# Kernel tuning notes

Hardware: AMD Instinct MI355X
Metric: run time of the kernel (lower is better)

Reference implementation:

```python
import jax, jax.numpy as jnp
import numpy as np

B, C, H, W = 16, 1, 128, 8192
N_MAX = 128
CHIRP_W, PERIOD = 48, 64
W_OUT = N_MAX * CHIRP_W + (N_MAX - 1)  # 6271 compacted columns (chirps + separators)
SEP_CLASS_ID = 2


def setup_inputs() -> dict:
    key = jax.random.key(0)
    k1, k2, k3, k4 = jax.random.split(key, 4)
    x = jax.random.normal(k1, (B, C, H, W), dtype=jnp.float32)
    starts = jnp.arange(N_MAX, dtype=jnp.int32) * PERIOD
    xi = jnp.stack([starts, starts + CHIRP_W], axis=-1)           # (N_MAX, 2)
    xi = jnp.broadcast_to(xi[None], (B, N_MAX, 2)).astype(jnp.int32)
    N = jax.random.randint(k2, (B,), 96, N_MAX + 1, dtype=jnp.int32)
    N = N.at[0].set(N_MAX)  # pin so static W_OUT equals torch's dynamic int(w_max.max())
    xl = jax.random.randint(k3, (B, W), 0, 2, dtype=jnp.int32)
    sep_param = jax.random.normal(k4, (1, 1, 1), dtype=jnp.float32)
    return {"x": x, "xi": xi, "N": N, "xl": xl, "sep_param": sep_param, "w_out": W_OUT}


def _compactify(x, xi, N, xl, sep_param, w_out):
    """Vectorized TinyBird.compactify_data: remove silence, keep chirp blocks,
    insert one separator column between consecutive valid chirps."""
    Bx, Cx, Hx, Wx = x.shape
    n_max = xi.shape[1]
    idx = jnp.arange(n_max, dtype=jnp.int32)[None, :]             # (1, N_max)
    Nb = N.reshape(-1, 1).astype(jnp.int32)
    valid = idx < Nb                                              # (B, N_max)

    s0, e0 = xi[..., 0], xi[..., 1]
    w = jnp.clip(e0 - s0, 0, None)
    w_valid = jnp.where(valid, w, 0)
    csum = jnp.cumsum(w_valid, axis=1)
    sn = csum - w_valid + idx                                     # new start (seps before = idx)
    en = csum + idx                                               # new end
    xi_new = jnp.where(valid[..., None], jnp.stack([sn, en], -1), 0).astype(xi.dtype)

    BIG = jnp.int32(1 << 30)
    en_srt = jnp.where(valid, en, BIG)                            # strictly increasing over valid part
    t = jnp.arange(w_out, dtype=jnp.int32)[None, :]               # (1, w_out)
    # i = number of chirp ends <= t  ->  chirp whose [sn_i, en_i) may contain t
    i = (en_srt[:, :, None] <= t[:, None, :]).sum(axis=1).astype(jnp.int32)  # (B, w_out)
    ic = jnp.clip(i, 0, n_max - 1)
    take = lambda a: jnp.take_along_axis(a, ic, axis=1)
    sn_i, en_i = take(sn), take(en)
    s0_i, e0_i = take(s0), take(e0)
    in_chirp = (i < Nb) & (t >= sn_i) & (en_i > sn_i) & (e0_i > s0_i)
    src = jnp.clip(s0_i + (t - sn_i), 0, Wx - 1)                  # (B, w_out)

    # separator column: t == en_{i-1}, previous chirp is not the last valid one, en < W
    jp = jnp.clip(i - 1, 0, n_max - 1)
    en_prev = jnp.take_along_axis(en, jp, axis=1)
    is_sep = (i >= 1) & (t == en_prev) & ((i - 1) < (Nb - 1)) & (en_prev < Wx)

    x_g = jnp.take_along_axis(x, src[:, None, None, :], axis=3)   # (B, C, H, w_out)
    sep = sep_param[0, 0, 0]
    x_new = jnp.where(in_chirp[:, None, None, :], x_g,
                      jnp.where(is_sep[:, None, None, :], sep, jnp.float32(0)))
    xl_g = jnp.take_along_axis(xl, src, axis=1)
    xl_new = jnp.where(in_chirp, xl_g,
                       jnp.where(is_sep, jnp.asarray(SEP_CLASS_ID, xl.dtype),
                                 jnp.asarray(0, xl.dtype)))
    return x_new, xi_new, xl_new


def reference(x, xi, N, xl, sep_param, w_out):
    return _compactify(x, xi, N, xl, sep_param, w_out)
```

## Files before the change

### kernel.cpp

```cpp
#include <hip/hip_runtime.h>

#define BB     16
#define HH     128
#define WW     8192
#define N_MAXC 128
#define W_OUTC 6271
#define SEP_CLASS 2.0f

#define X_ELEMS (BB * HH * W_OUTC)
#define XI_OFF  (X_ELEMS)
#define XL_OFF  (X_ELEMS + BB * N_MAXC * 2)
#define NCHUNKS (X_ELEMS / 4)

#define MAP_BYTES ((size_t)(BB * W_OUTC) * sizeof(int))

#define GBLK  1568
#define GSTR  (GBLK * 256)
#define GITER 8

#define MTILE 512

__global__ __launch_bounds__(256) void tb_meta(const int* __restrict__ xi,
                                               const int* __restrict__ Nv,
                                               const int* __restrict__ xl,
                                               float* __restrict__ out,
                                               int* __restrict__ map) {
    __shared__ int s_s0[N_MAXC], s_e0[N_MAXC], s_scan[N_MAXC], s_sn[N_MAXC], s_en[N_MAXC];
    const int b   = blockIdx.x;
    const int tid = threadIdx.x;
    const int Nb  = Nv[b];

    int wv = 0;
    if (tid < N_MAXC) {
        int2 se = ((const int2*)xi)[b * N_MAXC + tid];
        s_s0[tid] = se.x; s_e0[tid] = se.y;
        int w = se.y - se.x; if (w < 0) w = 0;
        wv = (tid < Nb) ? w : 0;
        s_scan[tid] = wv;
    }
    __syncthreads();
    #pragma unroll
    for (int off = 1; off < N_MAXC; off <<= 1) {
        int v = 0;
        if (tid < N_MAXC && tid >= off) v = s_scan[tid - off];
        __syncthreads();
        if (tid < N_MAXC) s_scan[tid] += v;
        __syncthreads();
    }
    if (tid < N_MAXC) {
        int c = s_scan[tid];
        s_sn[tid] = c - wv + tid;
        s_en[tid] = c + tid;
    }
    __syncthreads();

    if (blockIdx.y == 0 && tid < N_MAXC) {
        const bool valid = tid < Nb;
        out[XI_OFF + (b * N_MAXC + tid) * 2 + 0] = valid ? (float)s_sn[tid] : 0.0f;
        out[XI_OFF + (b * N_MAXC + tid) * 2 + 1] = valid ? (float)s_en[tid] : 0.0f;
    }

    const int t_lo = blockIdx.y * MTILE;
    const int t_hi = (t_lo + MTILE < W_OUTC) ? t_lo + MTILE : W_OUTC;
    for (int t = t_lo + tid; t < t_hi; t += 256) {
        int lo = 0, hi = Nb;
        while (lo < hi) { int mid = (lo + hi) >> 1; if (s_en[mid] <= t) lo = mid + 1; else hi = mid; }
        const int i  = lo;
        const int ic = (i < N_MAXC - 1) ? i : (N_MAXC - 1);
        int m = -2;
        if (i < Nb) {
            int sn = s_sn[ic], en = s_en[ic];
            if (t >= sn && en > sn && s_e0[ic] > s_s0[ic]) {
                int src = s_s0[ic] + (t - sn);
                src = src < 0 ? 0 : (src > WW - 1 ? WW - 1 : src);
                m = src;
            }
        }
        if (m == -2 && i >= 1) {
            int ep = s_en[i - 1];
            if (t == ep && (i - 1) < (Nb - 1) && ep < WW) m = -1;
        }
        if (map) map[b * W_OUTC + t] = m;
        float v = (m >= 0) ? (float)xl[b * WW + m] : ((m == -1) ? SEP_CLASS : 0.0f);
        out[XL_OFF + b * W_OUTC + t] = v;
    }
}

__global__ __launch_bounds__(256) void tb_gather_flat(const float* __restrict__ x,
                                                      const int* __restrict__ map,
                                                      const float* __restrict__ sep_param,
                                                      float* __restrict__ out) {
    const unsigned gtid = blockIdx.x * 256u + threadIdx.x;
    const float sep = sep_param[0];

    unsigned rowA[GITER], colA[GITER];
    int      mv[GITER][4];
    float    xv[GITER][4];

    #pragma unroll
    for (int j = 0; j < GITER; ++j) {
        unsigned c = gtid + (unsigned)j * (unsigned)GSTR;
        if (c >= (unsigned)NCHUNKS) c = NCHUNKS - 1;
        const unsigned flat = c * 4u;
        const unsigned bh   = flat / (unsigned)W_OUTC;
        rowA[j] = bh;
        colA[j] = flat - bh * (unsigned)W_OUTC;
    }
    #pragma unroll
    for (int j = 0; j < GITER; ++j) {
        #pragma unroll
        for (int k = 0; k < 4; ++k) {
            unsigned tk = colA[j] + (unsigned)k;
            unsigned r  = rowA[j];
            if (tk >= (unsigned)W_OUTC) { tk -= (unsigned)W_OUTC; r += 1u; }
            mv[j][k] = map[(r >> 7) * (unsigned)W_OUTC + tk];
        }
    }
    #pragma unroll
    for (int j = 0; j < GITER; ++j) {
        #pragma unroll
        for (int k = 0; k < 4; ++k) {
            unsigned tk = colA[j] + (unsigned)k;
            unsigned r  = rowA[j];
            if (tk >= (unsigned)W_OUTC) r += 1u;
            const int m = mv[j][k];
            const unsigned a = (m >= 0) ? (unsigned)m : 0u;
            xv[j][k] = x[((size_t)r << 13) + a];
        }
    }
    #pragma unroll
    for (int j = 0; j < GITER; ++j) {
        const unsigned c = gtid + (unsigned)j * (unsigned)GSTR;
        if (c < (unsigned)NCHUNKS) {
            float4 v;
            v.x = (mv[j][0] >= 0) ? xv[j][0] : ((mv[j][0] == -1) ? sep : 0.0f);
            v.y = (mv[j][1] >= 0) ? xv[j][1] : ((mv[j][1] == -1) ? sep : 0.0f);
            v.z = (mv[j][2] >= 0) ? xv[j][2] : ((mv[j][2] == -1) ? sep : 0.0f);
            v.w = (mv[j][3] >= 0) ? xv[j][3] : ((mv[j][3] == -1) ? sep : 0.0f);
            ((float4*)out)[c] = v;
        }
    }
}

#define FTILE   512
#define FHCHUNK 32

__global__ __launch_bounds__(256) void tb_gather_tiled(const float* __restrict__ x,
                                                       const int* __restrict__ xi,
                                                       const int* __restrict__ Nv,
                                                       const float* __restrict__ sep_param,
                                                       float* __restrict__ out) {
    __shared__ int s_s0[N_MAXC], s_e0[N_MAXC], s_sn[N_MAXC], s_en[N_MAXC];
    __shared__ int s_map[FTILE];
    const int b = blockIdx.z, h0 = blockIdx.y * FHCHUNK, t0 = blockIdx.x * FTILE;
    const int tid = threadIdx.x, Nb = Nv[b];
    if (tid < N_MAXC) {
        s_s0[tid] = xi[(b * N_MAXC + tid) * 2 + 0];
        s_e0[tid] = xi[(b * N_MAXC + tid) * 2 + 1];
    }
    __syncthreads();
    if (tid == 0) {
        int c = 0;
        for (int i = 0; i < N_MAXC; ++i) {
            int w = s_e0[i] - s_s0[i]; if (w < 0) w = 0;
            int wvv = (i < Nb) ? w : 0;
            c += wvv;
            s_sn[i] = c - wvv + i;
            s_en[i] = c + i;
        }
    }
    __syncthreads();
    for (int j = tid; j < FTILE; j += 256) {
        int t = t0 + j, m = -2;
        if (t < W_OUTC) {
            int lo = 0, hi = Nb;
            while (lo < hi) { int mid = (lo + hi) >> 1; if (s_en[mid] <= t) lo = mid + 1; else hi = mid; }
            int i = lo, ic = (i < N_MAXC - 1) ? i : (N_MAXC - 1);
            if (i < Nb) {
                int sn = s_sn[ic], en = s_en[ic];
                if (t >= sn && en > sn && s_e0[ic] > s_s0[ic]) {
                    int src = s_s0[ic] + (t - sn);
                    m = src < 0 ? 0 : (src > WW - 1 ? WW - 1 : src);
                }
            }
            if (m == -2 && i >= 1) {
                int ep = s_en[i - 1];
                if (t == ep && (i - 1) < (Nb - 1) && ep < WW) m = -1;
            }
        }
        s_map[j] = m;
    }
    __syncthreads();
    const float sep = sep_param[0];
    const float* xb = x + (size_t)b * HH * WW;
    float* ob = out + (size_t)b * HH * W_OUTC;
    for (int r = 0; r < FHCHUNK; ++r) {
        const int h = h0 + r;
        const float* xr = xb + (size_t)h * WW;
        float* orow = ob + (size_t)h * W_OUTC;
        for (int j = tid; j < FTILE; j += 256) {
            int t = t0 + j;
            if (t < W_OUTC) {
                int m = s_map[j];
                orow[t] = (m >= 0) ? xr[m] : ((m == -1) ? sep : 0.0f);
            }
        }
    }
}

extern "C" void kernel_launch(void* const* d_in, const int* in_sizes, int n_in,
                              void* d_out, int out_size, void* d_ws, size_t ws_size,
                              hipStream_t stream) {
    const float* x   = (const float*)d_in[0];
    const int*   xi  = (const int*)  d_in[1];
    const int*   Nv  = (const int*)  d_in[2];
    const int*   xl  = (const int*)  d_in[3];
    const float* sep = (const float*)d_in[4];
    float*       out = (float*)d_out;

    const bool use_ws = (ws_size >= MAP_BYTES) && (d_ws != nullptr);
    int* map = use_ws ? (int*)d_ws : nullptr;

    tb_meta<<<dim3(BB, 13), dim3(256), 0, stream>>>(xi, Nv, xl, out, map);

    if (use_ws) {
        tb_gather_flat<<<dim3(GBLK), dim3(256), 0, stream>>>(x, map, sep, out);
    } else {
        dim3 grid((W_OUTC + FTILE - 1) / FTILE, HH / FHCHUNK, BB);
        tb_gather_tiled<<<grid, dim3(256), 0, stream>>>(x, xi, Nv, sep, out);
    }
}
```

Before: 135.6 us.

## Stage per-batch column map in LDS and gather per batch with nontemporal stores

Replaces the flat grid-strided gather with a kernel launched over a (chunk, batch) grid. Each block copies its batch's column map into shared memory with vector loads, then reads map entries from LDS instead of global memory. The map row is padded to 6272 so the vector copy stays aligned, and output is written with nontemporal float4 stores. The aim is to cut repeated global map traffic and cache pollution from streaming writes, at the cost of about 25 KB of LDS per block, which may limit occupancy.

New measurement: 127.2 us. -6.2%, faster.

```diff
diff --git a/kernel.cpp b/kernel.cpp
--- a/kernel.cpp
+++ b/kernel.cpp
@@ -5,20 +5,25 @@
 #define WW     8192
 #define N_MAXC 128
 #define W_OUTC 6271
+#define MROW   6272
 #define SEP_CLASS 2.0f
 
 #define X_ELEMS (BB * HH * W_OUTC)
 #define XI_OFF  (X_ELEMS)
 #define XL_OFF  (X_ELEMS + BB * N_MAXC * 2)
-#define NCHUNKS (X_ELEMS / 4)
-
-#define MAP_BYTES ((size_t)(BB * W_OUTC) * sizeof(int))
-
-#define GBLK  1568
-#define GSTR  (GBLK * 256)
-#define GITER 8
+
+#define BATCH_ELEMS  (HH * W_OUTC)
+#define BATCH_CHUNKS (BATCH_ELEMS / 4)
+#define RPB   128
+#define CPB   1568
+#define KPT   7
+
+#define MAP_BYTES ((size_t)(BB * MROW) * sizeof(int))
 
 #define MTILE 512
+
+typedef float  vf4 __attribute__((ext_vector_type(4)));
+typedef int    vi4 __attribute__((ext_vector_type(4)));
 
 __global__ __launch_bounds__(256) void tb_meta(const int* __restrict__ xi,
                                                const int* __restrict__ Nv,
@@ -80,64 +85,76 @@
             int ep = s_en[i - 1];
             if (t == ep && (i - 1) < (Nb - 1) && ep < WW) m = -1;
         }
-        if (map) map[b * W_OUTC + t] = m;
+        if (map) map[b * MROW + t] = m;
         float v = (m >= 0) ? (float)xl[b * WW + m] : ((m == -1) ? SEP_CLASS : 0.0f);
         out[XL_OFF + b * W_OUTC + t] = v;
     }
 }
 
-__global__ __launch_bounds__(256) void tb_gather_flat(const float* __restrict__ x,
-                                                      const int* __restrict__ map,
-                                                      const float* __restrict__ sep_param,
-                                                      float* __restrict__ out) {
-    const unsigned gtid = blockIdx.x * 256u + threadIdx.x;
+__global__ __launch_bounds__(256) void tb_gather_lds(const float* __restrict__ x,
+                                                     const int* __restrict__ map,
+                                                     const float* __restrict__ sep_param,
+                                                     float* __restrict__ out) {
+    __shared__ __align__(16) int s_map[MROW];
+    const int b   = blockIdx.y;
+    const int r   = blockIdx.x;
+    const int tid = threadIdx.x;
+
+    const vi4* msrc = (const vi4*)(map + (size_t)b * MROW);
+    #pragma unroll
+    for (int k = 0; k < 7; ++k) {
+        int idx = tid + k * 256;
+        if (idx < MROW / 4) ((vi4*)s_map)[idx] = msrc[idx];
+    }
+    __syncthreads();
+
     const float sep = sep_param[0];
-
-    unsigned rowA[GITER], colA[GITER];
-    int      mv[GITER][4];
-    float    xv[GITER][4];
-
-    #pragma unroll
-    for (int j = 0; j < GITER; ++j) {
-        unsigned c = gtid + (unsigned)j * (unsigned)GSTR;
-        if (c >= (unsigned)NCHUNKS) c = NCHUNKS - 1;
-        const unsigned flat = c * 4u;
-        const unsigned bh   = flat / (unsigned)W_OUTC;
-        rowA[j] = bh;
-        colA[j] = flat - bh * (unsigned)W_OUTC;
-    }
-    #pragma unroll
-    for (int j = 0; j < GITER; ++j) {
+    const int   c0  = r * CPB;
+    const float* xb = x   + ((size_t)b << 20);
+    float*       ob = out + (size_t)b * BATCH_ELEMS;
+
+    unsigned hh[KPT], tt[KPT];
+    int   mv[KPT][4];
+    float xv[KPT][4];
+    bool  act[KPT];
+
+    #pragma unroll
+    for (int k = 0; k < KPT; ++k) {
+        int cl = c0 + tid + k * 256;
+        act[k] = (tid + k * 256 < CPB) && (cl < BATCH_CHUNKS);
+        if (!act[k]) cl = 0;
+        const unsigned e = (unsigned)cl * 4u;
+        const unsigned h = e / (unsigned)W_OUTC;
+        const unsigned t = e - h * (unsigned)W_OUTC;
+        hh[k] = h; tt[k] = t;
         #pragma unroll
-        for (int k = 0; k < 4; ++k) {
-            unsigned tk = colA[j] + (unsigned)k;
-            unsigned r  = rowA[j];
-            if (tk >= (unsigned)W_OUTC) { tk -= (unsigned)W_OUTC; r += 1u; }
-            mv[j][k] = map[(r >> 7) * (unsigned)W_OUTC + tk];
-        }
-    }
-    #pragma unroll
-    for (int j = 0; j < GITER; ++j) {
+        for (int kk = 0; kk < 4; ++kk) {
+            unsigned tk = t + (unsigned)kk;
+            if (tk >= (unsigned)W_OUTC) tk -= (unsigned)W_OUTC;
+            mv[k][kk] = s_map[tk];
+        }
+    }
+    #pragma unroll
+    for (int k = 0; k < KPT; ++k) {
         #pragma unroll
-        for (int k = 0; k < 4; ++k) {
-            unsigned tk = colA[j] + (unsigned)k;
-            unsigned r  = rowA[j];
-            if (tk >= (unsigned)W_OUTC) r += 1u;
-            const int m = mv[j][k];
+        for (int kk = 0; kk < 4; ++kk) {
+            unsigned tk = tt[k] + (unsigned)kk;
+            unsigned h  = hh[k] + ((tk >= (unsigned)W_OUTC) ? 1u : 0u);
+            const int m = mv[k][kk];
             const unsigned a = (m >= 0) ? (unsigned)m : 0u;
-            xv[j][k] = x[((size_t)r << 13) + a];
-        }
-    }
-    #pragma unroll
-    for (int j = 0; j < GITER; ++j) {
-        const unsigned c = gtid + (unsigned)j * (unsigned)GSTR;
-        if (c < (unsigned)NCHUNKS) {
-            float4 v;
-            v.x = (mv[j][0] >= 0) ? xv[j][0] : ((mv[j][0] == -1) ? sep : 0.0f);
-            v.y = (mv[j][1] >= 0) ? xv[j][1] : ((mv[j][1] == -1) ? sep : 0.0f);
-            v.z = (mv[j][2] >= 0) ? xv[j][2] : ((mv[j][2] == -1) ? sep : 0.0f);
-            v.w = (mv[j][3] >= 0) ? xv[j][3] : ((mv[j][3] == -1) ? sep : 0.0f);
-            ((float4*)out)[c] = v;
+            xv[k][kk] = xb[((size_t)h << 13) + a];
+        }
+    }
+    #pragma unroll
+    for (int k = 0; k < KPT; ++k) {
+        if (act[k]) {
+            const int cl = c0 + tid + k * 256;
+            vf4 v;
+            v.x = (mv[k][0] >= 0) ? xv[k][0] : ((mv[k][0] == -1) ? sep : 0.0f);
+            v.y = (mv[k][1] >= 0) ? xv[k][1] : ((mv[k][1] == -1) ? sep : 0.0f);
+            v.z = (mv[k][2] >= 0) ? xv[k][2] : ((mv[k][2] == -1) ? sep : 0.0f);
+            v.w = (mv[k][3] >= 0) ? xv[k][3] : ((mv[k][3] == -1) ? sep : 0.0f);
+            __builtin_nontemporal_store(v, ((vf4*)ob) + cl);
         }
     }
 }
@@ -224,7 +241,7 @@
     tb_meta<<<dim3(BB, 13), dim3(256), 0, stream>>>(xi, Nv, xl, out, map);
 
     if (use_ws) {
-        tb_gather_flat<<<dim3(GBLK), dim3(256), 0, stream>>>(x, map, sep, out);
+        tb_gather_lds<<<dim3(RPB, BB), dim3(256), 0, stream>>>(x, map, sep, out);
     } else {
         dim3 grid((W_OUTC + FTILE - 1) / FTILE, HH / FHCHUNK, BB);
         tb_gather_tiled<<<grid, dim3(256), 0, stream>>>(x, xi, Nv, sep, out);
```

## Fuse metadata and gather into one tiled kernel with per-block column map

Applied to the files above, without the earlier changes.

Replaces the two-kernel design (meta kernel writing a global column map, then a flat gather kernel reading it) with a single kernel. Each block of 512 columns by 16 rows by batch recomputes the chirp scan and column map into shared memory. The map round-trip through global memory and one launch are removed. In exchange the scan and binary search are repeated in every block, and output stores become four scalar writes per thread, since rows of 6271 floats are not 16-byte aligned.

Result: faster. 126.1 us (-7.0%).

```diff
diff --git a/kernel.cpp b/kernel.cpp
--- a/kernel.cpp
+++ b/kernel.cpp
@@ -10,23 +10,25 @@
 #define X_ELEMS (BB * HH * W_OUTC)
 #define XI_OFF  (X_ELEMS)
 #define XL_OFF  (X_ELEMS + BB * N_MAXC * 2)
-#define NCHUNKS (X_ELEMS / 4)
 
-#define MAP_BYTES ((size_t)(BB * W_OUTC) * sizeof(int))
+#define TCOLS 512
+#define HROWS 16
+#define NTILE 13
 
-#define GBLK  1568
-#define GSTR  (GBLK * 256)
-#define GITER 8
+typedef int vi4 __attribute__((ext_vector_type(4)));
 
-#define MTILE 512
+__global__ __launch_bounds__(256, 4) void tb_fused(const float* __restrict__ x,
+                                                   const int* __restrict__ xi,
+                                                   const int* __restrict__ Nv,
+                                                   const int* __restrict__ xl,
+                                                   const float* __restrict__ sep_param,
+                                                   float* __restrict__ out) {
+    __shared__ int s_s0[N_MAXC], s_e0[N_MAXC], s_scan[N_MAXC], s_sn[N_MAXC], s_en[N_MAXC];
+    __shared__ __align__(16) int s_map[TCOLS];
 
-__global__ __launch_bounds__(256) void tb_meta(const int* __restrict__ xi,
-                                               const int* __restrict__ Nv,
-                                               const int* __restrict__ xl,
-                                               float* __restrict__ out,
-                                               int* __restrict__ map) {
-    __shared__ int s_s0[N_MAXC], s_e0[N_MAXC], s_scan[N_MAXC], s_sn[N_MAXC], s_en[N_MAXC];
-    const int b   = blockIdx.x;
+    const int t0  = blockIdx.x * TCOLS;
+    const int h0  = blockIdx.y * HROWS;
+    const int b   = blockIdx.z;
     const int tid = threadIdx.x;
     const int Nb  = Nv[b];
 
@@ -54,128 +56,16 @@
     }
     __syncthreads();
 
-    if (blockIdx.y == 0 && tid < N_MAXC) {
-        const bool valid = tid < Nb;
-        out[XI_OFF + (b * N_MAXC + tid) * 2 + 0] = valid ? (float)s_sn[tid] : 0.0f;
-        out[XI_OFF + (b * N_MAXC + tid) * 2 + 1] = valid ? (float)s_en[tid] : 0.0f;
-    }
-
-    const int t_lo = blockIdx.y * MTILE;
-    const int t_hi = (t_lo + MTILE < W_OUTC) ? t_lo + MTILE : W_OUTC;
-    for (int t = t_lo + tid; t < t_hi; t += 256) {
-        int lo = 0, hi = Nb;
-        while (lo < hi) { int mid = (lo + hi) >> 1; if (s_en[mid] <= t) lo = mid + 1; else hi = mid; }
-        const int i  = lo;
-        const int ic = (i < N_MAXC - 1) ? i : (N_MAXC - 1);
+    #pragma unroll
+    for (int q = 0; q < 2; ++q) {
+        const int j = tid + q * 256;
+        const int t = t0 + j;
         int m = -2;
-        if (i < Nb) {
-            int sn = s_sn[ic], en = s_en[ic];
-            if (t >= sn && en > sn && s_e0[ic] > s_s0[ic]) {
-                int src = s_s0[ic] + (t - sn);
-                src = src < 0 ? 0 : (src > WW - 1 ? WW - 1 : src);
-                m = src;
-            }
-        }
-        if (m == -2 && i >= 1) {
-            int ep = s_en[i - 1];
-            if (t == ep && (i - 1) < (Nb - 1) && ep < WW) m = -1;
-        }
-        if (map) map[b * W_OUTC + t] = m;
-        float v = (m >= 0) ? (float)xl[b * WW + m] : ((m == -1) ? SEP_CLASS : 0.0f);
-        out[XL_OFF + b * W_OUTC + t] = v;
-    }
-}
-
-__global__ __launch_bounds__(256) void tb_gather_flat(const float* __restrict__ x,
-                                                      const int* __restrict__ map,
-                                                      const float* __restrict__ sep_param,
-                                                      float* __restrict__ out) {
-    const unsigned gtid = blockIdx.x * 256u + threadIdx.x;
-    const float sep = sep_param[0];
-
-    unsigned rowA[GITER], colA[GITER];
-    int      mv[GITER][4];
-    float    xv[GITER][4];
-
-    #pragma unroll
-    for (int j = 0; j < GITER; ++j) {
-        unsigned c = gtid + (unsigned)j * (unsigned)GSTR;
-        if (c >= (unsigned)NCHUNKS) c = NCHUNKS - 1;
-        const unsigned flat = c * 4u;
-        const unsigned bh   = flat / (unsigned)W_OUTC;
-        rowA[j] = bh;
-        colA[j] = flat - bh * (unsigned)W_OUTC;
-    }
-    #pragma unroll
-    for (int j = 0; j < GITER; ++j) {
-        #pragma unroll
-        for (int k = 0; k < 4; ++k) {
-            unsigned tk = colA[j] + (unsigned)k;
-            unsigned r  = rowA[j];
-            if (tk >= (unsigned)W_OUTC) { tk -= (unsigned)W_OUTC; r += 1u; }
-            mv[j][k] = map[(r >> 7) * (unsigned)W_OUTC + tk];
-        }
-    }
-    #pragma unroll
-    for (int j = 0; j < GITER; ++j) {
-        #pragma unroll
-        for (int k = 0; k < 4; ++k) {
-            unsigned tk = colA[j] + (unsigned)k;
-            unsigned r  = rowA[j];
-            if (tk >= (unsigned)W_OUTC) r += 1u;
-            const int m = mv[j][k];
-            const unsigned a = (m >= 0) ? (unsigned)m : 0u;
-            xv[j][k] = x[((size_t)r << 13) + a];
-        }
-    }
-    #pragma unroll
-    for (int j = 0; j < GITER; ++j) {
-        const unsigned c = gtid + (unsigned)j * (unsigned)GSTR;
-        if (c < (unsigned)NCHUNKS) {
-            float4 v;
-            v.x = (mv[j][0] >= 0) ? xv[j][0] : ((mv[j][0] == -1) ? sep : 0.0f);
-            v.y = (mv[j][1] >= 0) ? xv[j][1] : ((mv[j][1] == -1) ? sep : 0.0f);
-            v.z = (mv[j][2] >= 0) ? xv[j][2] : ((mv[j][2] == -1) ? sep : 0.0f);
-            v.w = (mv[j][3] >= 0) ? xv[j][3] : ((mv[j][3] == -1) ? sep : 0.0f);
-            ((float4*)out)[c] = v;
-        }
-    }
-}
-
-#define FTILE   512
-#define FHCHUNK 32
-
-__global__ __launch_bounds__(256) void tb_gather_tiled(const float* __restrict__ x,
-                                                       const int* __restrict__ xi,
-                                                       const int* __restrict__ Nv,
-                                                       const float* __restrict__ sep_param,
-                                                       float* __restrict__ out) {
-    __shared__ int s_s0[N_MAXC], s_e0[N_MAXC], s_sn[N_MAXC], s_en[N_MAXC];
-    __shared__ int s_map[FTILE];
-    const int b = blockIdx.z, h0 = blockIdx.y * FHCHUNK, t0 = blockIdx.x * FTILE;
-    const int tid = threadIdx.x, Nb = Nv[b];
-    if (tid < N_MAXC) {
-        s_s0[tid] = xi[(b * N_MAXC + tid) * 2 + 0];
-        s_e0[tid] = xi[(b * N_MAXC + tid) * 2 + 1];
-    }
-    __syncthreads();
-    if (tid == 0) {
-        int c = 0;
-        for (int i = 0; i < N_MAXC; ++i) {
-            int w = s_e0[i] - s_s0[i]; if (w < 0) w = 0;
-            int wvv = (i < Nb) ? w : 0;
-            c += wvv;
-            s_sn[i] = c - wvv + i;
-            s_en[i] = c + i;
-        }
-    }
-    __syncthreads();
-    for (int j = tid; j < FTILE; j += 256) {
-        int t = t0 + j, m = -2;
         if (t < W_OUTC) {
             int lo = 0, hi = Nb;
             while (lo < hi) { int mid = (lo + hi) >> 1; if (s_en[mid] <= t) lo = mid + 1; else hi = mid; }
-            int i = lo, ic = (i < N_MAXC - 1) ? i : (N_MAXC - 1);
+            const int i  = lo;
+            const int ic = (i < N_MAXC - 1) ? i : (N_MAXC - 1);
             if (i < Nb) {
                 int sn = s_sn[ic], en = s_en[ic];
                 if (t >= sn && en > sn && s_e0[ic] > s_s0[ic]) {
@@ -190,20 +80,67 @@
         }
         s_map[j] = m;
     }
+
+    if (blockIdx.y == 0 && blockIdx.x == 0 && tid < N_MAXC) {
+        const bool valid = tid < Nb;
+        out[XI_OFF + (b * N_MAXC + tid) * 2 + 0] = valid ? (float)s_sn[tid] : 0.0f;
+        out[XI_OFF + (b * N_MAXC + tid) * 2 + 1] = valid ? (float)s_en[tid] : 0.0f;
+    }
     __syncthreads();
+
+    if (blockIdx.y == 0) {
+        #pragma unroll
+        for (int q = 0; q < 2; ++q) {
+            const int j = tid + q * 256;
+            const int t = t0 + j;
+            if (t < W_OUTC) {
+                const int m = s_map[j];
+                float v = (m >= 0) ? (float)xl[b * WW + m] : ((m == -1) ? SEP_CLASS : 0.0f);
+                out[XL_OFF + b * W_OUTC + t] = v;
+            }
+        }
+    }
+
     const float sep = sep_param[0];
-    const float* xb = x + (size_t)b * HH * WW;
-    float* ob = out + (size_t)b * HH * W_OUTC;
-    for (int r = 0; r < FHCHUNK; ++r) {
-        const int h = h0 + r;
-        const float* xr = xb + (size_t)h * WW;
-        float* orow = ob + (size_t)h * W_OUTC;
-        for (int j = tid; j < FTILE; j += 256) {
-            int t = t0 + j;
-            if (t < W_OUTC) {
-                int m = s_map[j];
-                orow[t] = (m >= 0) ? xr[m] : ((m == -1) ? sep : 0.0f);
-            }
+    const int   c   = tid & 127;
+    const int   rb  = tid >> 7;
+    const vi4   mv  = ((const vi4*)s_map)[c];
+    const int   tA  = t0 + 4 * c;
+
+    const float* xb = x   + ((size_t)b << 20);
+    float*       ob = out + (size_t)b * (HH * W_OUTC);
+
+    const unsigned a0 = (mv.x >= 0) ? (unsigned)mv.x : 0u;
+    const unsigned a1 = (mv.y >= 0) ? (unsigned)mv.y : 0u;
+    const unsigned a2 = (mv.z >= 0) ? (unsigned)mv.z : 0u;
+    const unsigned a3 = (mv.w >= 0) ? (unsigned)mv.w : 0u;
+    const float f0 = (mv.x == -1) ? sep : 0.0f;
+    const float f1 = (mv.y == -1) ? sep : 0.0f;
+    const float f2 = (mv.z == -1) ? sep : 0.0f;
+    const float f3 = (mv.w == -1) ? sep : 0.0f;
+
+    if (tA + 3 < W_OUTC) {
+        #pragma unroll
+        for (int rr = 0; rr < HROWS / 2; ++rr) {
+            const int h = h0 + rb + rr * 2;
+            const float* xr = xb + ((size_t)h << 13);
+            float* orow = ob + (size_t)h * W_OUTC + tA;
+            const float v0 = (mv.x >= 0) ? xr[a0] : f0;
+            const float v1 = (mv.y >= 0) ? xr[a1] : f1;
+            const float v2 = (mv.z >= 0) ? xr[a2] : f2;
+            const float v3 = (mv.w >= 0) ? xr[a3] : f3;
+            orow[0] = v0; orow[1] = v1; orow[2] = v2; orow[3] = v3;
+        }
+    } else if (tA < W_OUTC) {
+        const int nrem = W_OUTC - tA;
+        #pragma unroll
+        for (int rr = 0; rr < HROWS / 2; ++rr) {
+            const int h = h0 + rb + rr * 2;
+            const float* xr = xb + ((size_t)h << 13);
+            float* orow = ob + (size_t)h * W_OUTC + tA;
+            if (nrem > 0) orow[0] = (mv.x >= 0) ? xr[a0] : f0;
+            if (nrem > 1) orow[1] = (mv.y >= 0) ? xr[a1] : f1;
+            if (nrem > 2) orow[2] = (mv.z >= 0) ? xr[a2] : f2;
         }
     }
 }
@@ -218,15 +155,6 @@
     const float* sep = (const float*)d_in[4];
     float*       out = (float*)d_out;
 
-    const bool use_ws = (ws_size >= MAP_BYTES) && (d_ws != nullptr);
-    int* map = use_ws ? (int*)d_ws : nullptr;
-
-    tb_meta<<<dim3(BB, 13), dim3(256), 0, stream>>>(xi, Nv, xl, out, map);
-
-    if (use_ws) {
-        tb_gather_flat<<<dim3(GBLK), dim3(256), 0, stream>>>(x, map, sep, out);
-    } else {
-        dim3 grid((W_OUTC + FTILE - 1) / FTILE, HH / FHCHUNK, BB);
-        tb_gather_tiled<<<grid, dim3(256), 0, stream>>>(x, xi, Nv, sep, out);
-    }
+    dim3 grid(NTILE, HH / HROWS, BB);
+    tb_fused<<<grid, dim3(256), 0, stream>>>(x, xi, Nv, xl, sep, out);
 }
```
